# Performance work log

Hardware: AMD Instinct MI355X
Metric: run time of the kernel (lower is better)

The kernel has to match this reference:

```python
import jax, jax.numpy as jnp
import numpy as np

N, E, H, R, C = 20000, 640000, 256, 10, 7
B, MAXLEN = 64, 110


def setup_inputs() -> dict:
    key = jax.random.key(0)
    ks = jax.random.split(key, 12)
    return {
        "speaker": jax.random.randint(ks[0], (N,), 0, 2),
        "x": jax.random.normal(ks[1], (N, H), dtype=jnp.float32),
        "edge_index": jax.random.randint(ks[2], (2, E), 0, N),
        "edge_norm": jax.random.uniform(ks[3], (E,), dtype=jnp.float32),
        "edge_type": jax.random.randint(ks[4], (E,), 0, R),
        "seq_lengths": jax.random.randint(ks[5], (B,), 1, MAXLEN),
        "umask": jnp.ones((B, MAXLEN), dtype=jnp.float32),
        "w1": jax.random.normal(ks[6], (R, H, H), dtype=jnp.float32) * 0.02,
        "w2": jax.random.normal(ks[7], (R, H, H), dtype=jnp.float32) * 0.02,
        "lin_W": jax.random.normal(ks[8], (2 * H, H), dtype=jnp.float32) * 0.02,
        "lin_b": jnp.zeros((H,), dtype=jnp.float32),
        "fc_W": jax.random.normal(ks[9], (H, C), dtype=jnp.float32) * 0.02,
        "fc_b": jnp.zeros((C,), dtype=jnp.float32),
    }


def gnn_layer(x, w, edge_index, edge_type, edge_norm):
    # PyG MessagePassing with flow='target_to_source', aggr='mean':
    #   x_j = x[edge_index[1]], aggregate at i = edge_index[0]
    i, j = edge_index[0], edge_index[1]
    # per-edge msg = x_j @ w[edge_type]; compute as relation-batched GEMM
    xw = jnp.einsum('nd,rdo->rno', x, w)          # [R, N, H]
    msgs = xw[edge_type, j] * edge_norm[:, None]   # [E, H]
    sums = jax.ops.segment_sum(msgs, i, num_segments=x.shape[0])
    cnt = jax.ops.segment_sum(jnp.ones_like(edge_norm), i, num_segments=x.shape[0])
    return sums / jnp.maximum(cnt, 1.0)[:, None]   # scatter-mean (0 for isolated nodes)


def reference(speaker, x, edge_index, edge_norm, edge_type, seq_lengths, umask,
              w1, w2, lin_W, lin_b, fc_W, fc_b):
    en = edge_norm * 2.0  # forward passes edge_norm * 2
    # both GNN layers are type 'GGCN' -> update() returns aggr_out (GRU path is dead)
    out1 = jax.nn.sigmoid(gnn_layer(x, w1, edge_index, edge_type, en))  # dropout = eval identity
    out2 = gnn_layer(out1, w2, edge_index, edge_type, en)
    emotions = jnp.concatenate([x, out2], axis=1)            # [N, 2H]
    hidden = jax.nn.relu(emotions @ lin_W + lin_b)           # [N, H]
    logits = hidden @ fc_W + fc_b                            # [N, C]
    log_prob = jax.nn.log_softmax(logits, axis=1)
    return (log_prob, x, emotions)
```

## Files before the change

### kernel.cpp

```cpp
#include <hip/hip_runtime.h>

typedef short bf16x8 __attribute__((ext_vector_type(8)));
typedef float f32x4 __attribute__((ext_vector_type(4)));

#define RH 2560

__device__ __forceinline__ unsigned short f2bf(float f) {
  unsigned u = __float_as_uint(f);
  u += 0x7fffu + ((u >> 16) & 1u);
  return (unsigned short)(u >> 16);
}
__device__ __forceinline__ float bf2f(unsigned short s) {
  return __uint_as_float(((unsigned)s) << 16);
}

__global__ void zero_int(int* __restrict__ p, int n) {
  int i = blockIdx.x * 256 + threadIdx.x;
  if (i < n) p[i] = 0;
}
__global__ void hist_kernel(const int* __restrict__ ei, const int* __restrict__ ety,
                            int E, int* __restrict__ cnt) {
  int e = blockIdx.x * 256 + threadIdx.x;
  if (e < E) atomicAdd(&cnt[ei[e] * 10 + ety[e]], 1);
}

__global__ __launch_bounds__(1024) void scan_local(const int* __restrict__ cnt,
                                                   int* __restrict__ offs,
                                                   int* __restrict__ bsum, int n) {
  __shared__ int ps[1024];
  const int t = threadIdx.x;
  const int base = blockIdx.x * 4096 + t * 4;
  int v0 = (base + 0 < n) ? cnt[base + 0] : 0;
  int v1 = (base + 1 < n) ? cnt[base + 1] : 0;
  int v2 = (base + 2 < n) ? cnt[base + 2] : 0;
  int v3 = (base + 3 < n) ? cnt[base + 3] : 0;
  int s = v0 + v1 + v2 + v3;
  ps[t] = s;
  __syncthreads();
  for (int off = 1; off < 1024; off <<= 1) {
    int add = (t >= off) ? ps[t - off] : 0;
    __syncthreads();
    ps[t] += add;
    __syncthreads();
  }
  int run = t ? ps[t - 1] : 0;
  if (base + 0 < n) offs[base + 0] = run; run += v0;
  if (base + 1 < n) offs[base + 1] = run; run += v1;
  if (base + 2 < n) offs[base + 2] = run; run += v2;
  if (base + 3 < n) offs[base + 3] = run;
  if (t == 1023) bsum[blockIdx.x] = ps[1023];
}
__global__ __launch_bounds__(1024) void scan_bsum(int* __restrict__ bsum,
                                                  int* __restrict__ offs,
                                                  int nb, int n) {
  __shared__ int ps[1024];
  const int t = threadIdx.x;
  int v = (t < nb) ? bsum[t] : 0;
  ps[t] = v;
  __syncthreads();
  for (int off = 1; off < 1024; off <<= 1) {
    int add = (t >= off) ? ps[t - off] : 0;
    __syncthreads();
    ps[t] += add;
    __syncthreads();
  }
  if (t < nb) bsum[t] = ps[t] - v;
  if (t == nb - 1) offs[n] = ps[t];
}
__global__ __launch_bounds__(1024) void scan_add(int* __restrict__ offs,
                                                 const int* __restrict__ bsum, int n) {
  const int add = bsum[blockIdx.x];
  const int base = blockIdx.x * 4096 + threadIdx.x * 4;
#pragma unroll
  for (int k = 0; k < 4; ++k) {
    int idx = base + k;
    if (idx < n) offs[idx] += add;
  }
}

__global__ void copy_int(const int* __restrict__ a, int* __restrict__ b, int n) {
  int i = blockIdx.x * 256 + threadIdx.x;
  if (i < n) b[i] = a[i];
}
__global__ void scatter_kernel(const int* __restrict__ ei, const int* __restrict__ ejj,
                               const int* __restrict__ ety, const float* __restrict__ enm,
                               int E, int* __restrict__ cursor, int2* __restrict__ jnpk) {
  int e = blockIdx.x * 256 + threadIdx.x;
  if (e < E) {
    int s = atomicAdd(&cursor[ei[e] * 10 + ety[e]], 1);
    jnpk[s] = make_int2(ejj[e], __float_as_int(enm[e] * 2.0f));
  }
}

__global__ void packW(const float* __restrict__ w, unsigned short* __restrict__ Wt) {
  int idx = blockIdx.x * 256 + threadIdx.x;
  if (idx >= 256 * RH) return;
  int o = idx / RH;
  int k = idx - o * RH;
  Wt[idx] = f2bf(w[(size_t)k * 256 + o]);
}
__global__ void packLin(const float* __restrict__ lw, unsigned short* __restrict__ Wt) {
  int idx = blockIdx.x * 256 + threadIdx.x;
  if (idx >= 256 * 512) return;
  int o = idx >> 9;
  int k = idx & 511;
  Wt[idx] = f2bf(lw[(size_t)k * 256 + o]);
}
__global__ void copyX(const float* __restrict__ x, float* __restrict__ xcopy,
                      float* __restrict__ em, unsigned short* __restrict__ em16,
                      unsigned short* __restrict__ x16, int total) {
  int idx = blockIdx.x * 256 + threadIdx.x;
  if (idx >= total) return;
  int nrow = idx >> 8, h = idx & 255;
  float v = x[idx];
  xcopy[idx] = v;
  em[(size_t)nrow * 512 + h] = v;
  em16[(size_t)nrow * 512 + h] = f2bf(v);
  x16[idx] = f2bf(v);
}

__global__ __launch_bounds__(256) void agg_kernel3(
    const unsigned short* __restrict__ src,
    const int* __restrict__ offs2,
    const int2* __restrict__ jnpk,
    unsigned short* __restrict__ S, int N)
{
  const int wave = threadIdx.x >> 6;
  const int lane = threadIdx.x & 63;
  const int node = blockIdx.x * 4 + wave;
  if (node >= N) return;
  const int b10 = node * 10;
  const int cb = lane * 4;
  float a0[10], a1[10], a2[10], a3[10];
#pragma unroll
  for (int r = 0; r < 10; ++r) {
    int sb = offs2[b10 + r];
    int se = offs2[b10 + r + 1];
    float b0 = 0.f, b1 = 0.f, b2 = 0.f, b3 = 0.f;
    for (int q = sb; q < se; ++q) {
      int2 jn = jnpk[q];
      float nr = __int_as_float(jn.y);
      uint2 v = *reinterpret_cast<const uint2*>(src + (size_t)jn.x * 256 + cb);
      b0 += nr * __uint_as_float(v.x << 16);
      b1 += nr * __uint_as_float(v.x & 0xffff0000u);
      b2 += nr * __uint_as_float(v.y << 16);
      b3 += nr * __uint_as_float(v.y & 0xffff0000u);
    }
    a0[r] = b0; a1[r] = b1; a2[r] = b2; a3[r] = b3;
  }
  int cc = offs2[b10 + 10] - offs2[b10];
  float scale = 1.0f / (float)(cc > 1 ? cc : 1);
  size_t base = (size_t)node * RH + cb;
#pragma unroll
  for (int r = 0; r < 10; ++r) {
    unsigned p0 = (unsigned)f2bf(a0[r] * scale) | ((unsigned)f2bf(a1[r] * scale) << 16);
    unsigned p1 = (unsigned)f2bf(a2[r] * scale) | ((unsigned)f2bf(a3[r] * scale) << 16);
    uint2 pk; pk.x = p0; pk.y = p1;
    *reinterpret_cast<uint2*>(S + base + r * 256) = pk;
  }
}

template<int MODE>
__global__ __launch_bounds__(256) void gemm128(
    const unsigned short* __restrict__ A,
    const unsigned short* __restrict__ Bt,
    int M, int K,
    float* __restrict__ fout,
    unsigned short* __restrict__ bout,
    const float* __restrict__ bias)
{
  __shared__ unsigned short At[128][40];
  __shared__ unsigned short Bs[128][40];
  const int tid = threadIdx.x;
  const int tileM = blockIdx.x * 128;
  const int tileN = blockIdx.y * 128;
  const int lane = tid & 63;
  const int wid = tid >> 6;
  const int wr = wid >> 1, wc = wid & 1;
  const int l15 = lane & 15, lq = lane >> 4;
  f32x4 acc[4][4] = {};
  const int nk = K >> 5;
  for (int kt = 0; kt < nk; ++kt) {
    __syncthreads();
#pragma unroll
    for (int p = 0; p < 2; ++p) {
      int c = tid + p * 256;
      int row = c >> 2;
      int ko = (c & 3) * 8;
      int gr = tileM + row;
      uint4 va = make_uint4(0u, 0u, 0u, 0u);
      if (gr < M) va = *reinterpret_cast<const uint4*>(A + (size_t)gr * K + kt * 32 + ko);
      *reinterpret_cast<uint4*>(&At[row][ko]) = va;
      uint4 vb = *reinterpret_cast<const uint4*>(Bt + (size_t)(tileN + row) * K + kt * 32 + ko);
      *reinterpret_cast<uint4*>(&Bs[row][ko]) = vb;
    }
    __syncthreads();
    bf16x8 af[4], bfr[4];
#pragma unroll
    for (int m = 0; m < 4; ++m)
      af[m] = *reinterpret_cast<const bf16x8*>(&At[wr * 64 + m * 16 + l15][lq * 8]);
#pragma unroll
    for (int n = 0; n < 4; ++n)
      bfr[n] = *reinterpret_cast<const bf16x8*>(&Bs[wc * 64 + n * 16 + l15][lq * 8]);
#pragma unroll
    for (int m = 0; m < 4; ++m)
#pragma unroll
      for (int n = 0; n < 4; ++n)
        acc[m][n] = __builtin_amdgcn_mfma_f32_16x16x32_bf16(af[m], bfr[n], acc[m][n], 0, 0, 0);
  }
  const int r0 = tileM + wr * 64;
  const int c0 = tileN + wc * 64;
#pragma unroll
  for (int m = 0; m < 4; ++m) {
#pragma unroll
    for (int n = 0; n < 4; ++n) {
      int col = c0 + n * 16 + l15;
      int rowb = r0 + m * 16 + lq * 4;
#pragma unroll
      for (int q = 0; q < 4; ++q) {
        int row = rowb + q;
        if (row < M) {
          float v = acc[m][n][q];
          if (MODE == 0) {
            float s = 1.0f / (1.0f + __expf(-v));
            bout[(size_t)row * 256 + col] = f2bf(s);
          } else if (MODE == 1) {
            fout[(size_t)row * 512 + col] = v;
            bout[(size_t)row * 512 + col] = f2bf(v);
          } else {
            float s = v + bias[col];
            s = s > 0.0f ? s : 0.0f;
            fout[(size_t)row * 256 + col] = s;
          }
        }
      }
    }
  }
}

__global__ __launch_bounds__(256) void fc_lsm(const float* __restrict__ hidden,
                                              const float* __restrict__ fcW,
                                              const float* __restrict__ fcb,
                                              float* __restrict__ outlp, int N) {
  __shared__ float hs[32 * 256];
  __shared__ float fw[256 * 7];
  __shared__ float lg[32][8];
  const int t = threadIdx.x;
  const int nb = blockIdx.x * 32;
  for (int c = t; c < 256 * 7; c += 256) fw[c] = fcW[c];
  for (int c = t; c < 32 * 256; c += 256) {
    int node = nb + (c >> 8);
    hs[c] = (node < N) ? hidden[(size_t)node * 256 + (c & 255)] : 0.0f;
  }
  __syncthreads();
  if (t < 224) {
    int ln = t / 7, c = t - ln * 7;
    float s = fcb[c];
    for (int h = 0; h < 256; ++h) s += hs[ln * 256 + h] * fw[h * 7 + c];
    lg[ln][c] = s;
  }
  __syncthreads();
  if (t < 32 && nb + t < N) {
    float m = lg[t][0];
    for (int c = 1; c < 7; ++c) m = fmaxf(m, lg[t][c]);
    float sum = 0.0f;
    for (int c = 0; c < 7; ++c) sum += __expf(lg[t][c] - m);
    float ls = __logf(sum);
    for (int c = 0; c < 7; ++c) outlp[(size_t)(nb + t) * 7 + c] = lg[t][c] - m - ls;
  }
}

extern "C" void kernel_launch(void* const* d_in, const int* in_sizes, int n_in,
                              void* d_out, int out_size, void* d_ws, size_t ws_size,
                              hipStream_t stream) {
  const float* x     = (const float*)d_in[1];
  const int*   ei    = (const int*)d_in[2];
  const float* enorm = (const float*)d_in[3];
  const int*   etype = (const int*)d_in[4];
  const float* w1    = (const float*)d_in[7];
  const float* w2    = (const float*)d_in[8];
  const float* linW  = (const float*)d_in[9];
  const float* linb  = (const float*)d_in[10];
  const float* fcW   = (const float*)d_in[11];
  const float* fcb   = (const float*)d_in[12];
  float* out = (float*)d_out;

  const int N = in_sizes[0];
  const int E = in_sizes[3];
  const int NB = N * 10;
  const int NSCAN = (NB + 4095) / 4096;

  char* ws = (char*)d_ws;
  size_t off = 0;
  auto carve = [&](size_t bytes) -> void* {
    void* p = ws + off;
    off += (bytes + 255) & ~(size_t)255;
    return p;
  };
  unsigned short* S    = (unsigned short*)carve((size_t)N * RH * 2);
  unsigned short* W1t  = (unsigned short*)carve((size_t)256 * RH * 2);
  unsigned short* W2t  = (unsigned short*)carve((size_t)256 * RH * 2);
  unsigned short* LWt  = (unsigned short*)carve((size_t)256 * 512 * 2);
  unsigned short* out1 = (unsigned short*)carve((size_t)N * 256 * 2);
  unsigned short* em16 = (unsigned short*)carve((size_t)N * 512 * 2);
  unsigned short* x16  = (unsigned short*)carve((size_t)N * 256 * 2);
  int* cnt2            = (int*)carve((size_t)NB * 4);
  int* offs2           = (int*)carve((size_t)(NB + 1) * 4);
  int* cursor          = (int*)carve((size_t)NB * 4);
  int* bsum            = (int*)carve((size_t)1024 * 4);
  int2* jnpk           = (int2*)carve((size_t)E * 8);
  float* hidden        = (float*)S;

  const int* e_i = ei;
  const int* e_j = ei + E;

  zero_int<<<(NB + 255) / 256, 256, 0, stream>>>(cnt2, NB);
  hist_kernel<<<(E + 255) / 256, 256, 0, stream>>>(e_i, etype, E, cnt2);
  scan_local<<<NSCAN, 1024, 0, stream>>>(cnt2, offs2, bsum, NB);
  scan_bsum<<<1, 1024, 0, stream>>>(bsum, offs2, NSCAN, NB);
  scan_add<<<NSCAN, 1024, 0, stream>>>(offs2, bsum, NB);
  copy_int<<<(NB + 255) / 256, 256, 0, stream>>>(offs2, cursor, NB);
  scatter_kernel<<<(E + 255) / 256, 256, 0, stream>>>(e_i, e_j, etype, enorm, E,
                                                      cursor, jnpk);

  packW<<<(256 * RH + 255) / 256, 256, 0, stream>>>(w1, W1t);
  packW<<<(256 * RH + 255) / 256, 256, 0, stream>>>(w2, W2t);
  packLin<<<(256 * 512 + 255) / 256, 256, 0, stream>>>(linW, LWt);
  copyX<<<((N * 256) + 255) / 256, 256, 0, stream>>>(
      x, out + (size_t)N * 7, out + (size_t)N * 263, em16, x16, N * 256);

  dim3 gemm_grid((N + 127) / 128, 2);

  agg_kernel3<<<(N + 3) / 4, 256, 0, stream>>>(x16, offs2, jnpk, S, N);
  gemm128<0><<<gemm_grid, 256, 0, stream>>>(S, W1t, N, RH, nullptr, out1, nullptr);

  agg_kernel3<<<(N + 3) / 4, 256, 0, stream>>>(out1, offs2, jnpk, S, N);
  gemm128<1><<<gemm_grid, 256, 0, stream>>>(S, W2t, N, RH,
      out + (size_t)N * 263 + 256, em16 + 256, nullptr);

  gemm128<2><<<gemm_grid, 256, 0, stream>>>(em16, LWt, N, 512, hidden, nullptr, linb);

  fc_lsm<<<(N + 31) / 32, 256, 0, stream>>>(hidden, fcW, fcb, out, N);
}
```

Measured before the change: 591.7 us.

## Split aggregation per (node,relation) bucket and shrink GEMM M-tile to 64

```diff
diff --git a/kernel.cpp b/kernel.cpp
--- a/kernel.cpp
+++ b/kernel.cpp
@@ -119,45 +119,53 @@
   x16[idx] = f2bf(v);
 }
 
-__global__ __launch_bounds__(256) void agg_kernel3(
+__global__ __launch_bounds__(256) void agg_bucket(
     const unsigned short* __restrict__ src,
     const int* __restrict__ offs2,
     const int2* __restrict__ jnpk,
-    unsigned short* __restrict__ S, int N)
+    unsigned short* __restrict__ S, int NB)
 {
-  const int wave = threadIdx.x >> 6;
+  const int bucket = blockIdx.x * 4 + (threadIdx.x >> 6);
+  if (bucket >= NB) return;
   const int lane = threadIdx.x & 63;
-  const int node = blockIdx.x * 4 + wave;
-  if (node >= N) return;
+  const int cb = lane * 4;
+  const int node = bucket / 10;
+  const int r = bucket - node * 10;
   const int b10 = node * 10;
-  const int cb = lane * 4;
-  float a0[10], a1[10], a2[10], a3[10];
-#pragma unroll
-  for (int r = 0; r < 10; ++r) {
-    int sb = offs2[b10 + r];
-    int se = offs2[b10 + r + 1];
-    float b0 = 0.f, b1 = 0.f, b2 = 0.f, b3 = 0.f;
-    for (int q = sb; q < se; ++q) {
-      int2 jn = jnpk[q];
-      float nr = __int_as_float(jn.y);
-      uint2 v = *reinterpret_cast<const uint2*>(src + (size_t)jn.x * 256 + cb);
-      b0 += nr * __uint_as_float(v.x << 16);
-      b1 += nr * __uint_as_float(v.x & 0xffff0000u);
-      b2 += nr * __uint_as_float(v.y << 16);
-      b3 += nr * __uint_as_float(v.y & 0xffff0000u);
-    }
-    a0[r] = b0; a1[r] = b1; a2[r] = b2; a3[r] = b3;
-  }
-  int cc = offs2[b10 + 10] - offs2[b10];
-  float scale = 1.0f / (float)(cc > 1 ? cc : 1);
-  size_t base = (size_t)node * RH + cb;
-#pragma unroll
-  for (int r = 0; r < 10; ++r) {
-    unsigned p0 = (unsigned)f2bf(a0[r] * scale) | ((unsigned)f2bf(a1[r] * scale) << 16);
-    unsigned p1 = (unsigned)f2bf(a2[r] * scale) | ((unsigned)f2bf(a3[r] * scale) << 16);
-    uint2 pk; pk.x = p0; pk.y = p1;
-    *reinterpret_cast<uint2*>(S + base + r * 256) = pk;
-  }
+  const int sb = offs2[bucket], se = offs2[bucket + 1];
+  const int cc = offs2[b10 + 10] - offs2[b10];
+  const float scale = 1.0f / (float)(cc > 1 ? cc : 1);
+  float b0 = 0.f, b1 = 0.f, b2 = 0.f, b3 = 0.f;
+  int q = sb;
+  for (; q + 2 <= se; q += 2) {
+    int2 e0 = jnpk[q];
+    int2 e1 = jnpk[q + 1];
+    float n0 = __int_as_float(e0.y);
+    float n1 = __int_as_float(e1.y);
+    uint2 v0 = *reinterpret_cast<const uint2*>(src + (size_t)e0.x * 256 + cb);
+    uint2 v1 = *reinterpret_cast<const uint2*>(src + (size_t)e1.x * 256 + cb);
+    b0 += n0 * __uint_as_float(v0.x << 16);
+    b1 += n0 * __uint_as_float(v0.x & 0xffff0000u);
+    b2 += n0 * __uint_as_float(v0.y << 16);
+    b3 += n0 * __uint_as_float(v0.y & 0xffff0000u);
+    b0 += n1 * __uint_as_float(v1.x << 16);
+    b1 += n1 * __uint_as_float(v1.x & 0xffff0000u);
+    b2 += n1 * __uint_as_float(v1.y << 16);
+    b3 += n1 * __uint_as_float(v1.y & 0xffff0000u);
+  }
+  if (q < se) {
+    int2 e0 = jnpk[q];
+    float n0 = __int_as_float(e0.y);
+    uint2 v0 = *reinterpret_cast<const uint2*>(src + (size_t)e0.x * 256 + cb);
+    b0 += n0 * __uint_as_float(v0.x << 16);
+    b1 += n0 * __uint_as_float(v0.x & 0xffff0000u);
+    b2 += n0 * __uint_as_float(v0.y << 16);
+    b3 += n0 * __uint_as_float(v0.y & 0xffff0000u);
+  }
+  unsigned p0 = (unsigned)f2bf(b0 * scale) | ((unsigned)f2bf(b1 * scale) << 16);
+  unsigned p1 = (unsigned)f2bf(b2 * scale) | ((unsigned)f2bf(b3 * scale) << 16);
+  uint2 pk; pk.x = p0; pk.y = p1;
+  *reinterpret_cast<uint2*>(S + (size_t)node * RH + r * 256 + cb) = pk;
 }
 
 template<int MODE>
@@ -169,49 +177,53 @@
     unsigned short* __restrict__ bout,
     const float* __restrict__ bias)
 {
-  __shared__ unsigned short At[128][40];
+  __shared__ unsigned short At[64][40];
   __shared__ unsigned short Bs[128][40];
   const int tid = threadIdx.x;
-  const int tileM = blockIdx.x * 128;
+  const int tileM = blockIdx.x * 64;
   const int tileN = blockIdx.y * 128;
   const int lane = tid & 63;
   const int wid = tid >> 6;
   const int wr = wid >> 1, wc = wid & 1;
   const int l15 = lane & 15, lq = lane >> 4;
-  f32x4 acc[4][4] = {};
+  f32x4 acc[2][4] = {};
   const int nk = K >> 5;
   for (int kt = 0; kt < nk; ++kt) {
     __syncthreads();
-#pragma unroll
-    for (int p = 0; p < 2; ++p) {
-      int c = tid + p * 256;
-      int row = c >> 2;
-      int ko = (c & 3) * 8;
+    {
+      int row = tid >> 2;
+      int ko = (tid & 3) * 8;
       int gr = tileM + row;
       uint4 va = make_uint4(0u, 0u, 0u, 0u);
       if (gr < M) va = *reinterpret_cast<const uint4*>(A + (size_t)gr * K + kt * 32 + ko);
       *reinterpret_cast<uint4*>(&At[row][ko]) = va;
-      uint4 vb = *reinterpret_cast<const uint4*>(Bt + (size_t)(tileN + row) * K + kt * 32 + ko);
-      *reinterpret_cast<uint4*>(&Bs[row][ko]) = vb;
+#pragma unroll
+      for (int p = 0; p < 2; ++p) {
+        int c = tid + p * 256;
+        int brow = c >> 2;
+        int bko = (c & 3) * 8;
+        uint4 vb = *reinterpret_cast<const uint4*>(Bt + (size_t)(tileN + brow) * K + kt * 32 + bko);
+        *reinterpret_cast<uint4*>(&Bs[brow][bko]) = vb;
+      }
     }
     __syncthreads();
-    bf16x8 af[4], bfr[4];
-#pragma unroll
-    for (int m = 0; m < 4; ++m)
-      af[m] = *reinterpret_cast<const bf16x8*>(&At[wr * 64 + m * 16 + l15][lq * 8]);
+    bf16x8 af[2], bfr[4];
+#pragma unroll
+    for (int m = 0; m < 2; ++m)
+      af[m] = *reinterpret_cast<const bf16x8*>(&At[wr * 32 + m * 16 + l15][lq * 8]);
 #pragma unroll
     for (int n = 0; n < 4; ++n)
       bfr[n] = *reinterpret_cast<const bf16x8*>(&Bs[wc * 64 + n * 16 + l15][lq * 8]);
 #pragma unroll
-    for (int m = 0; m < 4; ++m)
+    for (int m = 0; m < 2; ++m)
 #pragma unroll
       for (int n = 0; n < 4; ++n)
         acc[m][n] = __builtin_amdgcn_mfma_f32_16x16x32_bf16(af[m], bfr[n], acc[m][n], 0, 0, 0);
   }
-  const int r0 = tileM + wr * 64;
+  const int r0 = tileM + wr * 32;
   const int c0 = tileN + wc * 64;
 #pragma unroll
-  for (int m = 0; m < 4; ++m) {
+  for (int m = 0; m < 2; ++m) {
 #pragma unroll
     for (int n = 0; n < 4; ++n) {
       int col = c0 + n * 16 + l15;
@@ -329,12 +341,12 @@
   copyX<<<((N * 256) + 255) / 256, 256, 0, stream>>>(
       x, out + (size_t)N * 7, out + (size_t)N * 263, em16, x16, N * 256);
 
-  dim3 gemm_grid((N + 127) / 128, 2);
-
-  agg_kernel3<<<(N + 3) / 4, 256, 0, stream>>>(x16, offs2, jnpk, S, N);
+  dim3 gemm_grid((N + 63) / 64, 2);
+
+  agg_bucket<<<(NB + 3) / 4, 256, 0, stream>>>(x16, offs2, jnpk, S, NB);
   gemm128<0><<<gemm_grid, 256, 0, stream>>>(S, W1t, N, RH, nullptr, out1, nullptr);
 
-  agg_kernel3<<<(N + 3) / 4, 256, 0, stream>>>(out1, offs2, jnpk, S, N);
+  agg_bucket<<<(NB + 3) / 4, 256, 0, stream>>>(out1, offs2, jnpk, S, NB);
   gemm128<1><<<gemm_grid, 256, 0, stream>>>(S, W2t, N, RH,
       out + (size_t)N * 263 + 256, em16 + 256, nullptr);
 
```

New measurement: 521.8 us. 1.13x faster.
